# Kernel optimization log

Measured on AMD Instinct MI355X. Metric: run time of the kernel, lower is better.

Reference implementation:

```python
import jax, jax.numpy as jnp
import numpy as np

HEADS = 4

def _topk_mask(attn, k):
    # exact replica of mask.scatter_(-1, topk_indices, 1.0): exactly k ones per row
    C = attn.shape[-1]
    _, idx = jax.lax.top_k(attn, k)                      # [b,h,C,k]
    return jax.nn.one_hot(idx, C, dtype=attn.dtype).sum(axis=-2) > 0  # [b,h,C,C] bool


def setup_inputs() -> dict:
    key = jax.random.key(0)
    ks = jax.random.split(key, 8)
    b, dim, h, w = 32, 128, 4096, 1
    s = 0.05
    return {
        "x": jax.random.normal(ks[0], (b, dim, h, w), jnp.float32),
        "qkv_w": jax.random.normal(ks[1], (3 * dim, dim), jnp.float32) * s,
        "qkv_b": jax.random.normal(ks[2], (3 * dim,), jnp.float32) * s,
        "dw_w": jax.random.normal(ks[3], (3 * dim, 1, 3, 3), jnp.float32) * s,
        "dw_b": jax.random.normal(ks[4], (3 * dim,), jnp.float32) * s,
        "proj_w": jax.random.normal(ks[5], (dim, dim), jnp.float32) * s,
        "proj_b": jax.random.normal(ks[6], (dim,), jnp.float32) * s,
        "temperature": jnp.ones((HEADS, 1, 1), jnp.float32),
        "attn_w": jnp.full((4,), 0.2, jnp.float32),  # attn1..attn4
    }


def reference(x, qkv_w, qkv_b, dw_w, dw_b, proj_w, proj_b, temperature, attn_w):
    b, c, h, w = x.shape
    # 1x1 conv qkv, then 3x3 depthwise conv (groups = 3*c)
    qkv = jnp.einsum('bchw,oc->bohw', x, qkv_w) + qkv_b[None, :, None, None]
    qkv = jax.lax.conv_general_dilated(
        qkv, dw_w, window_strides=(1, 1), padding=((1, 1), (1, 1)),
        dimension_numbers=('NCHW', 'OIHW', 'NCHW'), feature_group_count=3 * c
    ) + dw_b[None, :, None, None]
    q, k, v = jnp.split(qkv, 3, axis=1)
    heads = lambda t: t.reshape(b, HEADS, c // HEADS, h * w)  # b head c (hw)
    q, k, v = heads(q), heads(k), heads(v)
    # F.normalize(dim=-1), eps=1e-12
    q = q / jnp.maximum(jnp.linalg.norm(q, axis=-1, keepdims=True), 1e-12)
    k = k / jnp.maximum(jnp.linalg.norm(k, axis=-1, keepdims=True), 1e-12)
    C = c // HEADS
    attn = jnp.einsum('bhcn,bhdn->bhcd', q, k) * temperature[None]  # [b,head,C,C]
    top_ks = [C // 2, (2 * C) // 3, (3 * C) // 4, (4 * C) // 5]
    out = jnp.zeros_like(v)
    for i, kk in enumerate(top_ks):
        m = _topk_mask(attn, kk)
        a = jax.nn.softmax(jnp.where(m, attn, -jnp.inf), axis=-1)
        out = out + attn_w[i] * jnp.einsum('bhcd,bhdn->bhcn', a, v)
    out = out.reshape(b, c, h, w)
    out = jnp.einsum('bchw,oc->bohw', out, proj_w) + proj_b[None, :, None, None]
    return out
```

## Files before the change

kernel.cpp:

```cpp
#include <hip/hip_runtime.h>

#define B_ 32
#define CD 128
#define O3 384
#define N  4096
#define H_ 4
#define C_ 32

typedef __bf16 bf16x8 __attribute__((ext_vector_type(8)));
typedef float floatx4 __attribute__((ext_vector_type(4)));

#define MFMA16(a, b, c) __builtin_amdgcn_mfma_f32_16x16x32_bf16(a, b, c, 0, 0, 0)

__device__ __forceinline__ float b2f(unsigned int u) {
  return __builtin_bit_cast(float, u << 16);
}
__device__ __forceinline__ float b2fh(unsigned int u) {
  return __builtin_bit_cast(float, u & 0xffff0000u);
}
__device__ __forceinline__ unsigned short f2b(float f) {
  unsigned int bits = __builtin_bit_cast(unsigned int, f);
  unsigned int r = (bits + 0x7FFFu + ((bits >> 16) & 1u)) >> 16;
  return (unsigned short)r;
}

__global__ __launch_bounds__(256) void k0_xt(
    const float* __restrict__ x, unsigned short* __restrict__ xT,
    const float* __restrict__ qkv_w, const float* __restrict__ proj_w,
    const float* __restrict__ dw_w, const float* __restrict__ dw_b,
    const float* __restrict__ qkv_b,
    unsigned short* __restrict__ qkv_wb, unsigned short* __restrict__ proj_wb,
    float4* __restrict__ dwq, float4* __restrict__ dwq2,
    float* __restrict__ c0a, float* __restrict__ c2a,
    float* __restrict__ part2)
{
  __shared__ float xt[32 * 68];
  const int t = threadIdx.x;
  const int n0 = blockIdx.x * 64, c0 = blockIdx.y * 32, b = blockIdx.z;
  const float* xb = x + ((size_t)b * CD + c0) * N + n0;
#pragma unroll
  for (int i = 0; i < 2; i++) {
    int f = i * 256 + t;
    int c = f >> 4, n4 = (f & 15) * 4;
    float4 v = *(const float4*)(xb + (size_t)c * N + n4);
    *(float4*)&xt[c * 68 + n4] = v;
  }

  if (blockIdx.z == 0 && blockIdx.y < 2) {
    int wid = blockIdx.y * 64 + blockIdx.x;
    if (wid < 66) {
      int e = (wid * 256 + t) * 4;
      if (e < 49152) {
        float4 v = *(const float4*)(qkv_w + e);
        unsigned short tmp[4] = {f2b(v.x), f2b(v.y), f2b(v.z), f2b(v.w)};
        *(uint2*)(qkv_wb + e) = *(uint2*)tmp;
      } else if (e < 65536) {
        int off = e - 49152;
        float4 v = *(const float4*)(proj_w + off);
        unsigned short tmp[4] = {f2b(v.x), f2b(v.y), f2b(v.z), f2b(v.w)};
        *(uint2*)(proj_wb + off) = *(uint2*)tmp;
      } else {
        int o = (e - 65536) >> 2;
        if (o < 384)
          dwq[o] = make_float4(dw_w[o * 9 + 1], dw_w[o * 9 + 4],
                               dw_w[o * 9 + 7], dw_b[o]);
      }
    } else if (wid == 66) {
      int o = t;
      float w0 = dw_w[o * 9 + 1], w1 = dw_w[o * 9 + 4], w2 = dw_w[o * 9 + 7];
      float qb = qkv_b[o];
      dwq2[o] = make_float4(w0, w1, w2, qb * (w0 + w1 + w2) + dw_b[o]);
      c0a[o] = qb * w0;
      c2a[o] = qb * w2;
    } else {
      int idx = (wid - 67) * 256 + t;
      uint4 z4 = make_uint4(0u, 0u, 0u, 0u);
      for (int k2 = idx; k2 < 34816; k2 += 61 * 256)
        ((uint4*)part2)[k2] = z4;
    }
  }

  __syncthreads();
  int n = t >> 2, cb = (t & 3) * 8;
  unsigned short tmp[8];
#pragma unroll
  for (int j = 0; j < 8; j++) tmp[j] = f2b(xt[(cb + j) * 68 + n]);
  *(uint4*)(xT + ((size_t)b * N + n0 + n) * CD + c0 + cb) = *(uint4*)tmp;
}

__global__ __launch_bounds__(256, 3) void k1_qkv_dw(
    const unsigned short* __restrict__ xT, const unsigned short* __restrict__ qkv_wb,
    const float* __restrict__ qkv_b, const float4* __restrict__ dwq,
    const float4* __restrict__ dwq2, const float* __restrict__ c0a,
    const float* __restrict__ c2a, unsigned short* __restrict__ vT,
    float* part2)
{
  __shared__ __align__(16) char smem[34816];
  const int t = threadIdx.x;
  const int b = blockIdx.y;
  const int wv = t >> 6, l = t & 63, quad = l >> 4, lm = l & 15;

  if (blockIdx.x < 67) {
    unsigned short* Bs    = (unsigned short*)smem;
    unsigned short* pres2 = (unsigned short*)smem;
    const int yw = blockIdx.x;
    const int ybase = yw * 62;
    const bool interior = (yw >= 1 && yw <= 65);

    const unsigned short* wbase = qkv_wb + (size_t)(wv * 64 + lm) * CD + quad * 8;
    bf16x8 wa[4][4];
#pragma unroll
    for (int mt = 0; mt < 4; mt++)
#pragma unroll
      for (int ks = 0; ks < 4; ks++)
        wa[mt][ks] = *(const bf16x8*)(wbase + (size_t)mt * 16 * CD + ks * 32);

    if (interior) {
#pragma unroll
      for (int i = 0; i < 4; i++) {
        int f = i * 256 + t;
        int row = f >> 4, c8 = (f & 15) * 8;
        *(uint4*)&Bs[row * 136 + c8] =
            *(const uint4*)(xT + ((size_t)b * N + ybase - 1 + row) * CD + c8);
      }
    } else {
#pragma unroll
      for (int i = 0; i < 4; i++) {
        int f = i * 256 + t;
        int row = f >> 4, c8 = (f & 15) * 8;
        int yg = ybase - 1 + row;
        uint4 v = make_uint4(0u, 0u, 0u, 0u);
        if (yg >= 0 && yg < N)
          v = *(const uint4*)(xT + ((size_t)b * N + yg) * CD + c8);
        *(uint4*)&Bs[row * 136 + c8] = v;
      }
    }
    __syncthreads();

    floatx4 acc[4][4];
#pragma unroll
    for (int mt = 0; mt < 4; mt++)
#pragma unroll
      for (int nt = 0; nt < 4; nt++) acc[mt][nt] = (floatx4){0.f, 0.f, 0.f, 0.f};

#pragma unroll
    for (int ks = 0; ks < 4; ks++) {
      bf16x8 bb[4];
#pragma unroll
      for (int nt = 0; nt < 4; nt++)
        bb[nt] = *(const bf16x8*)&Bs[(nt * 16 + lm) * 136 + ks * 32 + quad * 8];
#pragma unroll
      for (int mt = 0; mt < 4; mt++)
#pragma unroll
        for (int nt = 0; nt < 4; nt++)
          acc[mt][nt] = MFMA16(wa[mt][ks], bb[nt], acc[mt][nt]);
    }
    __syncthreads();

    const int i1 = (l & 48) | ((lm + 1) & 15);
    const int i2 = (l & 48) | ((lm + 2) & 15);
#pragma unroll
    for (int mt = 0; mt < 4; mt++) {
#pragma unroll
      for (int r = 0; r < 4; r++) {
        int o = wv * 64 + mt * 16 + quad * 4 + r;
        float4 wq = dwq2[o];
        float cc0 = 0.f, cc2 = 0.f;
        if (yw == 0)  cc0 = c0a[o];
        if (yw == 66) cc2 = c2a[o];
        float vv[5], r1[5], r2[5];
#pragma unroll
        for (int nt = 0; nt < 4; nt++) vv[nt] = acc[mt][nt][r];
        vv[4] = 0.f;
#pragma unroll
        for (int nt = 0; nt < 4; nt++) {
          r1[nt] = __shfl(vv[nt], i1);
          r2[nt] = __shfl(vv[nt], i2);
        }
        r1[4] = 0.f; r2[4] = 0.f;
#pragma unroll
        for (int nt = 0; nt < 4; nt++) {
          int p = nt * 16 + lm;
          int y = ybase + p;
          float g1 = (lm == 15) ? r1[nt + 1] : r1[nt];
          float g2 = (lm >= 14) ? r2[nt + 1] : r2[nt];
          float val = wq.x * vv[nt] + wq.y * g1 + wq.z * g2 + wq.w;
          if (y == 0)     val -= cc0;
          if (y == N - 1) val -= cc2;
          bool ok = (p < 62) && (y < N);
          pres2[o * 68 + p] = f2b(ok ? val : 0.f);
        }
      }
    }
    __syncthreads();

    const int h = wv;
    const unsigned short* pq = pres2 + (size_t)(h * 32) * 68;
    const unsigned short* pk = pres2 + (size_t)(128 + h * 32) * 68;
    floatx4 gqk[2][2], gqq[2], gkk[2];
#pragma unroll
    for (int a = 0; a < 2; a++) {
      gqq[a] = (floatx4){0.f, 0.f, 0.f, 0.f};
      gkk[a] = (floatx4){0.f, 0.f, 0.f, 0.f};
#pragma unroll
      for (int c = 0; c < 2; c++) gqk[a][c] = (floatx4){0.f, 0.f, 0.f, 0.f};
    }
#pragma unroll
    for (int kc = 0; kc < 2; kc++) {
      bf16x8 qf[2], kf[2];
#pragma unroll
      for (int tt = 0; tt < 2; tt++) {
        qf[tt] = *(const bf16x8*)&pq[(tt * 16 + lm) * 68 + kc * 32 + quad * 8];
        kf[tt] = *(const bf16x8*)&pk[(tt * 16 + lm) * 68 + kc * 32 + quad * 8];
      }
#pragma unroll
      for (int tq = 0; tq < 2; tq++)
#pragma unroll
        for (int tk = 0; tk < 2; tk++)
          gqk[tq][tk] = MFMA16(qf[tq], kf[tk], gqk[tq][tk]);
      gqq[0] = MFMA16(qf[0], qf[0], gqq[0]);
      gqq[1] = MFMA16(qf[1], qf[1], gqq[1]);
      gkk[0] = MFMA16(kf[0], kf[0], gkk[0]);
      gkk[1] = MFMA16(kf[1], kf[1], gkk[1]);
    }
    float* pp = part2 + ((size_t)b * H_ + h) * 1088;
#pragma unroll
    for (int tq = 0; tq < 2; tq++)
#pragma unroll
      for (int tk = 0; tk < 2; tk++)
#pragma unroll
        for (int r = 0; r < 4; r++)
          atomicAdd(&pp[(tq * 16 + quad * 4 + r) * 32 + tk * 16 + lm],
                    gqk[tq][tk][r]);
    if (quad == (lm >> 2)) {
      int r = lm & 3;
      atomicAdd(&pp[1024 + lm],      gqq[0][r]);
      atomicAdd(&pp[1024 + 16 + lm], gqq[1][r]);
      atomicAdd(&pp[1056 + lm],      gkk[0][r]);
      atomicAdd(&pp[1056 + 16 + lm], gkk[1][r]);
    }
  } else {
    unsigned short* Bs   = (unsigned short*)smem;
    unsigned short* pres = (unsigned short*)smem;
    const int ytile = blockIdx.x - 67;
    const int obase = 256;
    const int ybase = ytile * 124;
    const bool interior = (ytile >= 1 && ytile <= 32);

    const unsigned short* wbase =
        qkv_wb + (size_t)(obase + wv * 32 + lm) * CD + quad * 8;
    bf16x8 wa0[4], wa1[4];
#pragma unroll
    for (int ks = 0; ks < 4; ks++) {
      wa0[ks] = *(const bf16x8*)(wbase + ks * 32);
      wa1[ks] = *(const bf16x8*)(wbase + 16 * CD + ks * 32);
    }

    if (interior) {
#pragma unroll
      for (int i = 0; i < 8; i++) {
        int f = i * 256 + t;
        int row = f >> 4, c8 = (f & 15) * 8;
        *(uint4*)&Bs[row * 136 + c8] =
            *(const uint4*)(xT + ((size_t)b * N + ybase - 2 + row) * CD + c8);
      }
    } else {
#pragma unroll
      for (int i = 0; i < 8; i++) {
        int f = i * 256 + t;
        int row = f >> 4, c8 = (f & 15) * 8;
        int yg = ybase - 2 + row;
        uint4 v = make_uint4(0u, 0u, 0u, 0u);
        if (yg >= 0 && yg < N)
          v = *(const uint4*)(xT + ((size_t)b * N + yg) * CD + c8);
        *(uint4*)&Bs[row * 136 + c8] = v;
      }
    }
    __syncthreads();

    floatx4 acc[2][8];
#pragma unroll
    for (int mt = 0; mt < 2; mt++)
#pragma unroll
      for (int nt = 0; nt < 8; nt++) acc[mt][nt] = (floatx4){0.f, 0.f, 0.f, 0.f};

#pragma unroll
    for (int ks = 0; ks < 4; ks++) {
#pragma unroll
      for (int nt = 0; nt < 8; nt++) {
        bf16x8 bb = *(const bf16x8*)&Bs[(nt * 16 + lm) * 136 + ks * 32 + quad * 8];
        acc[0][nt] = MFMA16(wa0[ks], bb, acc[0][nt]);
        acc[1][nt] = MFMA16(wa1[ks], bb, acc[1][nt]);
      }
    }

    const int op = t & 63, quarter = t >> 6;
    const int o0 = 2 * op;
    const float4 wqa = dwq[256 + o0];
    const float4 wqb = dwq[256 + o0 + 1];
    __syncthreads();
    if (interior) {
#pragma unroll
      for (int mt = 0; mt < 2; mt++)
#pragma unroll
        for (int r = 0; r < 4; r++) {
          int o2 = wv * 32 + mt * 16 + quad * 4 + r;
          float bias = qkv_b[obase + o2];
#pragma unroll
          for (int nt = 0; nt < 8; nt++) {
            int i = nt * 16 + lm;
            pres[i * 132 + o2] = f2b(acc[mt][nt][r] + bias);
          }
        }
    } else {
#pragma unroll
      for (int mt = 0; mt < 2; mt++)
#pragma unroll
        for (int r = 0; r < 4; r++) {
          int o2 = wv * 32 + mt * 16 + quad * 4 + r;
          float bias = qkv_b[obase + o2];
#pragma unroll
          for (int nt = 0; nt < 8; nt++) {
            int i = nt * 16 + lm;
            int yg = ybase - 2 + i;
            pres[i * 132 + o2] =
                f2b((yg >= 0 && yg < N) ? (acc[mt][nt][r] + bias) : 0.f);
          }
        }
    }
    __syncthreads();
    const unsigned int* pu = (const unsigned int*)pres;
    int i0 = 2 + quarter * 31;
    unsigned int pm = pu[(i0 - 1) * 66 + op];
    unsigned int pc = pu[i0 * 66 + op];
    if (interior) {
      for (int i = i0; i < i0 + 31; i++) {
        unsigned int pp2 = pu[(i + 1) * 66 + op];
        int yo = ybase - 2 + i;
        float a0 = wqa.x * b2f(pm) + wqa.y * b2f(pc) + wqa.z * b2f(pp2) + wqa.w;
        float a1 = wqb.x * b2fh(pm) + wqb.y * b2fh(pc) + wqb.z * b2fh(pp2) + wqb.w;
        unsigned int pk2 = (unsigned int)f2b(a0) | ((unsigned int)f2b(a1) << 16);
        *(unsigned int*)(vT + ((size_t)b * N + yo) * CD + o0) = pk2;
        pm = pc; pc = pp2;
      }
    } else {
      for (int i = i0; i < i0 + 31; i++) {
        unsigned int pp2 = pu[(i + 1) * 66 + op];
        int yo = ybase - 2 + i;
        if (yo >= 0 && yo < N) {
          float a0 = wqa.x * b2f(pm) + wqa.y * b2f(pc) + wqa.z * b2f(pp2) + wqa.w;
          float a1 = wqb.x * b2fh(pm) + wqb.y * b2fh(pc) + wqb.z * b2fh(pp2) + wqb.w;
          unsigned int pk2 = (unsigned int)f2b(a0) | ((unsigned int)f2b(a1) << 16);
          *(unsigned int*)(vT + ((size_t)b * N + yo) * CD + o0) = pk2;
        }
        pm = pc; pc = pp2;
      }
    }
  }
}

__global__ __launch_bounds__(256) void k45(
    const float* __restrict__ part2, const unsigned short* __restrict__ proj_wb,
    const float* __restrict__ temperature, const float* __restrict__ attn_w,
    unsigned short* __restrict__ Mb)
{
  __shared__ float La[H_][C_][33];
  __shared__ float sq2[256];
  __shared__ float rn[256];
  __shared__ float exL[H_][C_][33];
  __shared__ unsigned char rkL[H_][C_][C_];
  __shared__ unsigned short AwtT[H_][C_][40];
  const int b = blockIdx.x, t = threadIdx.x;

  const float* pbb = part2 + (size_t)b * H_ * 1088;
#pragma unroll
  for (int h = 0; h < H_; h++)
    for (int idx = t; idx < 1088; idx += 256) {
      float s = pbb[h * 1088 + idx];
      if (idx < 1024) La[h][idx >> 5][idx & 31] = s;
      else if (idx < 1056) sq2[h * 32 + (idx - 1024)] = s;
      else sq2[128 + h * 32 + (idx - 1056)] = s;
    }
  __syncthreads();
  rn[t] = 1.f / fmaxf(sqrtf(sq2[t]), 1e-12f);
  __syncthreads();
  for (int e = t; e < 4096; e += 256) {
    int h = e >> 10, i = (e >> 5) & 31, j = e & 31;
    La[h][i][j] *= rn[h * 32 + i] * rn[128 + h * 32 + j] * temperature[h];
  }
  __syncthreads();

  if (t < 128) {
    int h = t >> 5, i = t & 31;
    float m = -1e30f;
    for (int j = 0; j < 32; j++) m = fmaxf(m, La[h][i][j]);
    float S0 = 0.f, S1 = 0.f, S2 = 0.f, S3 = 0.f;
    for (int j = 0; j < 32; j++) {
      float vj = La[h][i][j];
      int r = 0;
      for (int j2 = 0; j2 < 32; j2++) {
        float v2 = La[h][i][j2];
        r += (v2 > vj) || (v2 == vj && j2 < j);
      }
      float e = __expf(vj - m);
      exL[h][i][j] = e;
      rkL[h][i][j] = (unsigned char)r;
      if (r < 16) S0 += e;
      if (r < 21) S1 += e;
      if (r < 24) S2 += e;
      if (r < 25) S3 += e;
    }
    float w0 = attn_w[0] / S0, w1 = attn_w[1] / S1;
    float w2 = attn_w[2] / S2, w3 = attn_w[3] / S3;
    for (int j = 0; j < 32; j++) {
      int r = rkL[h][i][j];
      float cmb = (r < 16 ? w0 : 0.f) + (r < 21 ? w1 : 0.f) +
                  (r < 24 ? w2 : 0.f) + (r < 25 ? w3 : 0.f);
      AwtT[h][j][i] = f2b(exL[h][i][j] * cmb);
    }
  }
  __syncthreads();

  {
    const int wv = t >> 6, l = t & 63, quad = l >> 4, lm = l & 15;
    const int h = wv;
    bf16x8 bfr[2];
#pragma unroll
    for (int jt = 0; jt < 2; jt++)
      bfr[jt] = *(const bf16x8*)&AwtT[h][jt * 16 + lm][quad * 8];
#pragma unroll
    for (int mt = 0; mt < 8; mt++) {
      bf16x8 a = *(const bf16x8*)(proj_wb +
                    (size_t)(mt * 16 + lm) * CD + h * C_ + quad * 8);
#pragma unroll
      for (int jt = 0; jt < 2; jt++) {
        floatx4 acc = (floatx4){0.f, 0.f, 0.f, 0.f};
        acc = MFMA16(a, bfr[jt], acc);
#pragma unroll
        for (int r = 0; r < 4; r++) {
          int row = quad * 4 + r;
          Mb[(size_t)b * 16384 + (mt * 16 + row) * CD + h * C_ + jt * 16 + lm] =
              f2b(acc[r]);
        }
      }
    }
  }
}

__global__ __launch_bounds__(256, 4) void k6_out(
    const unsigned short* __restrict__ vT, const unsigned short* __restrict__ Mb,
    const float* __restrict__ proj_b, float* __restrict__ out)
{
  __shared__ unsigned short Bs[128 * 136];
  const int t = threadIdx.x;
  const int y0 = blockIdx.x * 128, b = blockIdx.y;
  const int wv = t >> 6, l = t & 63, quad = l >> 4, lm = l & 15;

#pragma unroll
  for (int i = 0; i < 8; i++) {
    int f = i * 256 + t;
    int row = f >> 4, c8 = (f & 15) * 8;
    *(uint4*)&Bs[row * 136 + c8] =
        *(const uint4*)(vT + ((size_t)b * N + y0 + row) * CD + c8);
  }
  __syncthreads();

  floatx4 acc[2][8];
#pragma unroll
  for (int mt = 0; mt < 2; mt++)
#pragma unroll
    for (int nt = 0; nt < 8; nt++) acc[mt][nt] = (floatx4){0.f, 0.f, 0.f, 0.f};

  const unsigned short* mbase =
      Mb + (size_t)b * 16384 + (size_t)(wv * 32 + lm) * CD + quad * 8;
#pragma unroll
  for (int ks = 0; ks < 4; ks++) {
    bf16x8 a0 = *(const bf16x8*)(mbase + ks * 32);
    bf16x8 a1 = *(const bf16x8*)(mbase + 16 * CD + ks * 32);
#pragma unroll
    for (int nt = 0; nt < 8; nt++) {
      bf16x8 bb = *(const bf16x8*)&Bs[(nt * 16 + lm) * 136 + ks * 32 + quad * 8];
      acc[0][nt] = MFMA16(a0, bb, acc[0][nt]);
      acc[1][nt] = MFMA16(a1, bb, acc[1][nt]);
    }
  }

#pragma unroll
  for (int mt = 0; mt < 2; mt++)
#pragma unroll
    for (int r = 0; r < 4; r++) {
      int o = wv * 32 + mt * 16 + quad * 4 + r;
      float pb = proj_b[o];
#pragma unroll
      for (int nt = 0; nt < 8; nt++) {
        int y = y0 + nt * 16 + lm;
        out[((size_t)b * CD + o) * N + y] = acc[mt][nt][r] + pb;
      }
    }
}

extern "C" void kernel_launch(void* const* d_in, const int* in_sizes, int n_in,
                              void* d_out, int out_size, void* d_ws, size_t ws_size,
                              hipStream_t stream)
{
  (void)in_sizes; (void)n_in; (void)out_size; (void)ws_size;
  const float* x           = (const float*)d_in[0];
  const float* qkv_w       = (const float*)d_in[1];
  const float* qkv_b       = (const float*)d_in[2];
  const float* dw_w        = (const float*)d_in[3];
  const float* dw_b        = (const float*)d_in[4];
  const float* proj_w      = (const float*)d_in[5];
  const float* proj_b      = (const float*)d_in[6];
  const float* temperature = (const float*)d_in[7];
  const float* attn_w      = (const float*)d_in[8];
  float* out = (float*)d_out;

  unsigned short* xT      = (unsigned short*)d_ws;
  unsigned short* qkv_wb  = xT + (size_t)16777216;
  unsigned short* proj_wb = qkv_wb + 49152;
  unsigned short* hole    = proj_wb + 16384;
  unsigned short* vT      = hole + (size_t)33554432;
  unsigned short* Mb      = vT + (size_t)16777216;
  float* part2 = (float*)(Mb + 524288);
  float4* dwq  = (float4*)Mb;
  float4* dwq2 = (float4*)(Mb + 3072);
  float*  c0a  = (float*)(Mb + 5120);
  float*  c2a  = (float*)(Mb + 5632);

  k0_xt    <<<dim3(64, 4, 32), 256, 0, stream>>>(x, xT, qkv_w, proj_w, dw_w,
                                                 dw_b, qkv_b, qkv_wb, proj_wb,
                                                 dwq, dwq2, c0a, c2a, part2);
  k1_qkv_dw<<<dim3(101, 32),   256, 0, stream>>>(xT, qkv_wb, qkv_b, dwq, dwq2,
                                                 c0a, c2a, vT, part2);
  k45      <<<dim3(B_),        256, 0, stream>>>(part2, proj_wb, temperature,
                                                 attn_w, Mb);
  k6_out   <<<dim3(32, B_),    256, 0, stream>>>(vT, Mb, proj_b, out);
}
```

Measured before the change: 234.9 us.

## Process two q/k windows per block and retile x transpose kernel

The q/k Gram-accumulation blocks now each handle two 62-row windows. Their weight fragments are loaded once per pair, and the partial Gram sums are accumulated in registers before a single set of atomics, which halves the atomic traffic and the weight reloads. The transpose kernel now reads all 128 channels for 32 positions per block and writes full 256-byte xT rows, with a padded stride of 33. The k1 occupancy hint is raised to 4 blocks per CU. The trade-off is fewer q/k blocks, so less parallelism, plus an extra barrier between the two windows.

```diff
diff --git a/kernel.cpp b/kernel.cpp
--- a/kernel.cpp
+++ b/kernel.cpp
@@ -34,20 +34,13 @@
     float* __restrict__ c0a, float* __restrict__ c2a,
     float* __restrict__ part2)
 {
-  __shared__ float xt[32 * 68];
+  __shared__ float xt[128 * 33];
   const int t = threadIdx.x;
-  const int n0 = blockIdx.x * 64, c0 = blockIdx.y * 32, b = blockIdx.z;
-  const float* xb = x + ((size_t)b * CD + c0) * N + n0;
-#pragma unroll
-  for (int i = 0; i < 2; i++) {
-    int f = i * 256 + t;
-    int c = f >> 4, n4 = (f & 15) * 4;
-    float4 v = *(const float4*)(xb + (size_t)c * N + n4);
-    *(float4*)&xt[c * 68 + n4] = v;
-  }
-
-  if (blockIdx.z == 0 && blockIdx.y < 2) {
-    int wid = blockIdx.y * 64 + blockIdx.x;
+  const int ns = blockIdx.x * 32, b = blockIdx.y;
+  const float* xb = x + (size_t)b * CD * N + ns;
+
+  if (blockIdx.y == 0) {
+    int wid = blockIdx.x;
     if (wid < 66) {
       int e = (wid * 256 + t) * 4;
       if (e < 49152) {
@@ -80,15 +73,27 @@
     }
   }
 
+#pragma unroll
+  for (int p = 0; p < 4; p++) {
+    int c = p * 32 + (t >> 3), n4 = (t & 7) * 4;
+    float4 v = *(const float4*)(xb + (size_t)c * N + n4);
+    float* dst = &xt[c * 33 + n4];
+    dst[0] = v.x; dst[1] = v.y; dst[2] = v.z; dst[3] = v.w;
+  }
   __syncthreads();
-  int n = t >> 2, cb = (t & 3) * 8;
+
+  const int n = t >> 3, cg = (t & 7) * 8;
   unsigned short tmp[8];
 #pragma unroll
-  for (int j = 0; j < 8; j++) tmp[j] = f2b(xt[(cb + j) * 68 + n]);
-  *(uint4*)(xT + ((size_t)b * N + n0 + n) * CD + c0 + cb) = *(uint4*)tmp;
-}
-
-__global__ __launch_bounds__(256, 3) void k1_qkv_dw(
+  for (int half = 0; half < 2; half++) {
+    int c8 = cg + half * 64;
+#pragma unroll
+    for (int j = 0; j < 8; j++) tmp[j] = f2b(xt[(c8 + j) * 33 + n]);
+    *(uint4*)(xT + ((size_t)b * N + ns + n) * CD + c8) = *(uint4*)tmp;
+  }
+}
+
+__global__ __launch_bounds__(256, 4) void k1_qkv_dw(
     const unsigned short* __restrict__ xT, const unsigned short* __restrict__ qkv_wb,
     const float* __restrict__ qkv_b, const float4* __restrict__ dwq,
     const float4* __restrict__ dwq2, const float* __restrict__ c0a,
@@ -100,12 +105,9 @@
   const int b = blockIdx.y;
   const int wv = t >> 6, l = t & 63, quad = l >> 4, lm = l & 15;
 
-  if (blockIdx.x < 67) {
+  if (blockIdx.x < 34) {
     unsigned short* Bs    = (unsigned short*)smem;
     unsigned short* pres2 = (unsigned short*)smem;
-    const int yw = blockIdx.x;
-    const int ybase = yw * 62;
-    const bool interior = (yw >= 1 && yw <= 65);
 
     const unsigned short* wbase = qkv_wb + (size_t)(wv * 64 + lm) * CD + quad * 8;
     bf16x8 wa[4][4];
@@ -115,88 +117,6 @@
       for (int ks = 0; ks < 4; ks++)
         wa[mt][ks] = *(const bf16x8*)(wbase + (size_t)mt * 16 * CD + ks * 32);
 
-    if (interior) {
-#pragma unroll
-      for (int i = 0; i < 4; i++) {
-        int f = i * 256 + t;
-        int row = f >> 4, c8 = (f & 15) * 8;
-        *(uint4*)&Bs[row * 136 + c8] =
-            *(const uint4*)(xT + ((size_t)b * N + ybase - 1 + row) * CD + c8);
-      }
-    } else {
-#pragma unroll
-      for (int i = 0; i < 4; i++) {
-        int f = i * 256 + t;
-        int row = f >> 4, c8 = (f & 15) * 8;
-        int yg = ybase - 1 + row;
-        uint4 v = make_uint4(0u, 0u, 0u, 0u);
-        if (yg >= 0 && yg < N)
-          v = *(const uint4*)(xT + ((size_t)b * N + yg) * CD + c8);
-        *(uint4*)&Bs[row * 136 + c8] = v;
-      }
-    }
-    __syncthreads();
-
-    floatx4 acc[4][4];
-#pragma unroll
-    for (int mt = 0; mt < 4; mt++)
-#pragma unroll
-      for (int nt = 0; nt < 4; nt++) acc[mt][nt] = (floatx4){0.f, 0.f, 0.f, 0.f};
-
-#pragma unroll
-    for (int ks = 0; ks < 4; ks++) {
-      bf16x8 bb[4];
-#pragma unroll
-      for (int nt = 0; nt < 4; nt++)
-        bb[nt] = *(const bf16x8*)&Bs[(nt * 16 + lm) * 136 + ks * 32 + quad * 8];
-#pragma unroll
-      for (int mt = 0; mt < 4; mt++)
-#pragma unroll
-        for (int nt = 0; nt < 4; nt++)
-          acc[mt][nt] = MFMA16(wa[mt][ks], bb[nt], acc[mt][nt]);
-    }
-    __syncthreads();
-
-    const int i1 = (l & 48) | ((lm + 1) & 15);
-    const int i2 = (l & 48) | ((lm + 2) & 15);
-#pragma unroll
-    for (int mt = 0; mt < 4; mt++) {
-#pragma unroll
-      for (int r = 0; r < 4; r++) {
-        int o = wv * 64 + mt * 16 + quad * 4 + r;
-        float4 wq = dwq2[o];
-        float cc0 = 0.f, cc2 = 0.f;
-        if (yw == 0)  cc0 = c0a[o];
-        if (yw == 66) cc2 = c2a[o];
-        float vv[5], r1[5], r2[5];
-#pragma unroll
-        for (int nt = 0; nt < 4; nt++) vv[nt] = acc[mt][nt][r];
-        vv[4] = 0.f;
-#pragma unroll
-        for (int nt = 0; nt < 4; nt++) {
-          r1[nt] = __shfl(vv[nt], i1);
-          r2[nt] = __shfl(vv[nt], i2);
-        }
-        r1[4] = 0.f; r2[4] = 0.f;
-#pragma unroll
-        for (int nt = 0; nt < 4; nt++) {
-          int p = nt * 16 + lm;
-          int y = ybase + p;
-          float g1 = (lm == 15) ? r1[nt + 1] : r1[nt];
-          float g2 = (lm >= 14) ? r2[nt + 1] : r2[nt];
-          float val = wq.x * vv[nt] + wq.y * g1 + wq.z * g2 + wq.w;
-          if (y == 0)     val -= cc0;
-          if (y == N - 1) val -= cc2;
-          bool ok = (p < 62) && (y < N);
-          pres2[o * 68 + p] = f2b(ok ? val : 0.f);
-        }
-      }
-    }
-    __syncthreads();
-
-    const int h = wv;
-    const unsigned short* pq = pres2 + (size_t)(h * 32) * 68;
-    const unsigned short* pk = pres2 + (size_t)(128 + h * 32) * 68;
     floatx4 gqk[2][2], gqq[2], gkk[2];
 #pragma unroll
     for (int a = 0; a < 2; a++) {
@@ -205,24 +125,118 @@
 #pragma unroll
       for (int c = 0; c < 2; c++) gqk[a][c] = (floatx4){0.f, 0.f, 0.f, 0.f};
     }
-#pragma unroll
-    for (int kc = 0; kc < 2; kc++) {
-      bf16x8 qf[2], kf[2];
-#pragma unroll
-      for (int tt = 0; tt < 2; tt++) {
-        qf[tt] = *(const bf16x8*)&pq[(tt * 16 + lm) * 68 + kc * 32 + quad * 8];
-        kf[tt] = *(const bf16x8*)&pk[(tt * 16 + lm) * 68 + kc * 32 + quad * 8];
-      }
-#pragma unroll
-      for (int tq = 0; tq < 2; tq++)
-#pragma unroll
-        for (int tk = 0; tk < 2; tk++)
-          gqk[tq][tk] = MFMA16(qf[tq], kf[tk], gqk[tq][tk]);
-      gqq[0] = MFMA16(qf[0], qf[0], gqq[0]);
-      gqq[1] = MFMA16(qf[1], qf[1], gqq[1]);
-      gkk[0] = MFMA16(kf[0], kf[0], gkk[0]);
-      gkk[1] = MFMA16(kf[1], kf[1], gkk[1]);
-    }
+    const int i1 = (l & 48) | ((lm + 1) & 15);
+    const int i2 = (l & 48) | ((lm + 2) & 15);
+    const int h = wv;
+
+    for (int w2 = 0; w2 < 2; w2++) {
+      const int win = blockIdx.x * 2 + w2;
+      if (win > 66) break;
+      const int ybase = win * 62;
+      const bool interior = (win >= 1 && win <= 65);
+
+      if (w2) __syncthreads();
+
+      if (interior) {
+#pragma unroll
+        for (int i = 0; i < 4; i++) {
+          int f = i * 256 + t;
+          int row = f >> 4, c8 = (f & 15) * 8;
+          *(uint4*)&Bs[row * 136 + c8] =
+              *(const uint4*)(xT + ((size_t)b * N + ybase - 1 + row) * CD + c8);
+        }
+      } else {
+#pragma unroll
+        for (int i = 0; i < 4; i++) {
+          int f = i * 256 + t;
+          int row = f >> 4, c8 = (f & 15) * 8;
+          int yg = ybase - 1 + row;
+          uint4 v = make_uint4(0u, 0u, 0u, 0u);
+          if (yg >= 0 && yg < N)
+            v = *(const uint4*)(xT + ((size_t)b * N + yg) * CD + c8);
+          *(uint4*)&Bs[row * 136 + c8] = v;
+        }
+      }
+      __syncthreads();
+
+      floatx4 acc[4][4];
+#pragma unroll
+      for (int mt = 0; mt < 4; mt++)
+#pragma unroll
+        for (int nt = 0; nt < 4; nt++)
+          acc[mt][nt] = (floatx4){0.f, 0.f, 0.f, 0.f};
+
+#pragma unroll
+      for (int ks = 0; ks < 4; ks++) {
+        bf16x8 bb[4];
+#pragma unroll
+        for (int nt = 0; nt < 4; nt++)
+          bb[nt] = *(const bf16x8*)&Bs[(nt * 16 + lm) * 136 + ks * 32 + quad * 8];
+#pragma unroll
+        for (int mt = 0; mt < 4; mt++)
+#pragma unroll
+          for (int nt = 0; nt < 4; nt++)
+            acc[mt][nt] = MFMA16(wa[mt][ks], bb[nt], acc[mt][nt]);
+      }
+      __syncthreads();
+
+#pragma unroll
+      for (int mt = 0; mt < 4; mt++) {
+#pragma unroll
+        for (int r = 0; r < 4; r++) {
+          int o = wv * 64 + mt * 16 + quad * 4 + r;
+          float4 wq = dwq2[o];
+          float cc0 = 0.f, cc2 = 0.f;
+          if (win == 0)  cc0 = c0a[o];
+          if (win == 66) cc2 = c2a[o];
+          float vv[5], r1[5], r2[5];
+#pragma unroll
+          for (int nt = 0; nt < 4; nt++) vv[nt] = acc[mt][nt][r];
+          vv[4] = 0.f;
+#pragma unroll
+          for (int nt = 0; nt < 4; nt++) {
+            r1[nt] = __shfl(vv[nt], i1);
+            r2[nt] = __shfl(vv[nt], i2);
+          }
+          r1[4] = 0.f; r2[4] = 0.f;
+#pragma unroll
+          for (int nt = 0; nt < 4; nt++) {
+            int p = nt * 16 + lm;
+            int y = ybase + p;
+            float g1 = (lm == 15) ? r1[nt + 1] : r1[nt];
+            float g2 = (lm >= 14) ? r2[nt + 1] : r2[nt];
+            float val = wq.x * vv[nt] + wq.y * g1 + wq.z * g2 + wq.w;
+            if (y == 0)     val -= cc0;
+            if (y == N - 1) val -= cc2;
+            bool ok = (p < 62) && (y < N);
+            pres2[o * 68 + p] = f2b(ok ? val : 0.f);
+          }
+        }
+      }
+      __syncthreads();
+
+      const unsigned short* pq = pres2 + (size_t)(h * 32) * 68;
+      const unsigned short* pk = pres2 + (size_t)(128 + h * 32) * 68;
+#pragma unroll
+      for (int kc = 0; kc < 2; kc++) {
+        bf16x8 qf[2], kf[2];
+#pragma unroll
+        for (int tt = 0; tt < 2; tt++) {
+          qf[tt] = *(const bf16x8*)&pq[(tt * 16 + lm) * 68 + kc * 32 + quad * 8];
+          kf[tt] = *(const bf16x8*)&pk[(tt * 16 + lm) * 68 + kc * 32 + quad * 8];
+        }
+#pragma unroll
+        for (int tq = 0; tq < 2; tq++)
+#pragma unroll
+          for (int tk = 0; tk < 2; tk++)
+            gqk[tq][tk] = MFMA16(qf[tq], kf[tk], gqk[tq][tk]);
+        gqq[0] = MFMA16(qf[0], qf[0], gqq[0]);
+        gqq[1] = MFMA16(qf[1], qf[1], gqq[1]);
+        gkk[0] = MFMA16(kf[0], kf[0], gkk[0]);
+        gkk[1] = MFMA16(kf[1], kf[1], gkk[1]);
+      }
+    }
+
     float* pp = part2 + ((size_t)b * H_ + h) * 1088;
 #pragma unroll
     for (int tq = 0; tq < 2; tq++)
@@ -242,7 +256,7 @@
   } else {
     unsigned short* Bs   = (unsigned short*)smem;
     unsigned short* pres = (unsigned short*)smem;
-    const int ytile = blockIdx.x - 67;
+    const int ytile = blockIdx.x - 34;
     const int obase = 256;
     const int ybase = ytile * 124;
     const bool interior = (ytile >= 1 && ytile <= 32);
@@ -527,12 +541,12 @@
   float*  c0a  = (float*)(Mb + 5120);
   float*  c2a  = (float*)(Mb + 5632);
 
-  k0_xt    <<<dim3(64, 4, 32), 256, 0, stream>>>(x, xT, qkv_w, proj_w, dw_w,
-                                                 dw_b, qkv_b, qkv_wb, proj_wb,
-                                                 dwq, dwq2, c0a, c2a, part2);
-  k1_qkv_dw<<<dim3(101, 32),   256, 0, stream>>>(xT, qkv_wb, qkv_b, dwq, dwq2,
-                                                 c0a, c2a, vT, part2);
-  k45      <<<dim3(B_),        256, 0, stream>>>(part2, proj_wb, temperature,
-                                                 attn_w, Mb);
-  k6_out   <<<dim3(32, B_),    256, 0, stream>>>(vT, Mb, proj_b, out);
-}
+  k0_xt    <<<dim3(128, 32),  256, 0, stream>>>(x, xT, qkv_w, proj_w, dw_w,
+                                                dw_b, qkv_b, qkv_wb, proj_wb,
+                                                dwq, dwq2, c0a, c2a, part2);
+  k1_qkv_dw<<<dim3(68, 32),   256, 0, stream>>>(xT, qkv_wb, qkv_b, dwq, dwq2,
+                                                c0a, c2a, vT, part2);
+  k45      <<<dim3(B_),       256, 0, stream>>>(part2, proj_wb, temperature,
+                                                attn_w, Mb);
+  k6_out   <<<dim3(32, B_),   256, 0, stream>>>(vT, Mb, proj_b, out);
+}
```

After: 303.9 us. 29.4% more time.
